# Optimization experiments

Hardware: AMD Instinct MI355X
Metric: run time of the kernel (lower is better)

Reference implementation:

```python
import jax, jax.numpy as jnp
import numpy as np

PATCH = 3      # forward default patch_size
ALPHA = 1.0    # forward default alpha
# scale_factor = 1 -> F.interpolate is the identity


def setup_inputs() -> dict:
    key = jax.random.key(0)
    x_l = jax.random.normal(key, (16, 1, 1536, 1536), dtype=jnp.float32)
    return {"x_l": x_l}


def reference(x_l):
    # x_l: [N, 1, H, W]
    N, C, H, W = x_l.shape
    p = PATCH
    pad = p // 2
    # zero-padded input, matching F.unfold's implicit zero padding
    xp = jnp.pad(x_l, ((0, 0), (0, 0), (pad, pad), (pad, pad)))
    # gather the p*p shifted views -> [N, p*p, H, W] (equivalent to F.unfold for C=1;
    # softmax + weighted sum over dim 1 is permutation-invariant over the patch axis)
    local = jnp.stack(
        [xp[:, 0, i:i + H, j:j + W] for i in range(p) for j in range(p)],
        axis=1,
    )
    # local_difference = local_l - x_l**2  (broadcast over the patch dim)
    diff = local - x_l[:, 0][:, None, :, :] ** 2
    corr = jax.nn.softmax(-diff / ALPHA, axis=1)
    # softmax-weighted local average -> [N, 1, H, W]
    return jnp.sum(corr * local, axis=1, keepdims=True)
```

## Files before the change

kernel.cpp:

```cpp
#include <hip/hip_runtime.h>
#include <math.h>

#define IMG_W 1536
#define IMG_H 1536
#define NIMG  16
#define RPB   32
#define NROWS (RPB + 2)
#define PF    6

typedef float f32x4 __attribute__((ext_vector_type(4)));

__global__ __launch_bounds__(128)
void WeightedAverage_55551107006568_kernel(const float* __restrict__ x,
                                           float* __restrict__ out) {
    const int g  = blockIdx.x * 128 + threadIdx.x;
    const int w0 = g << 2;
    const int h0 = blockIdx.y * RPB;
    const size_t plane = (size_t)blockIdx.z * ((size_t)IMG_H * IMG_W);
    const float* xp = x + plane;
    float* op = out + plane;

    const bool lok = (w0 > 0);
    const bool rok = (w0 + 4 < IMG_W);
    const int offL = lok ? -4 : 0;
    const int offR = rok ? 16 : 0;

    f32x4 m[NROWS];
    float hl[NROWS], hr[NROWS];

    auto issue = [&](int i) {
        const int r  = h0 - 1 + i;
        const int rc = r < 0 ? 0 : (r >= IMG_H ? IMG_H - 1 : r);
        const float* rp = xp + (size_t)rc * IMG_W + w0;
        m[i]  = *(const f32x4*)rp;
        hl[i] = *(const float*)((const char*)rp + offL);
        hr[i] = *(const float*)((const char*)rp + offR);
    };

#pragma unroll
    for (int i = 0; i < PF; ++i) issue(i);
    __builtin_amdgcn_sched_barrier(0);

    float hE[3][4], hVE[3][4];
#pragma unroll
    for (int i = 0; i < NROWS; ++i) {
        if (i + PF < NROWS) issue(i + PF);
        __builtin_amdgcn_sched_barrier(0);

        const int r  = h0 - 1 + i;
        const bool rv = (r >= 0) && (r < IMG_H);
        const int s = i % 3;

        f32x4 mm = m[i];
        float hlv = (rv && lok) ? hl[i] : 0.f;
        float hrv = (rv && rok) ? hr[i] : 0.f;
        if (!rv) mm = (f32x4){0.f, 0.f, 0.f, 0.f};

        const float eL = __expf(-hlv),  vL = hlv * eL;
        const float e0 = __expf(-mm.x), v0 = mm.x * e0;
        const float e1 = __expf(-mm.y), v1 = mm.y * e1;
        const float e2 = __expf(-mm.z), v2 = mm.z * e2;
        const float e3 = __expf(-mm.w), v3 = mm.w * e3;
        const float eR = __expf(-hrv),  vR = hrv * eR;
        hE[s][0] = eL + e0 + e1;  hVE[s][0] = vL + v0 + v1;
        hE[s][1] = e0 + e1 + e2;  hVE[s][1] = v0 + v1 + v2;
        hE[s][2] = e1 + e2 + e3;  hVE[s][2] = v1 + v2 + v3;
        hE[s][3] = e2 + e3 + eR;  hVE[s][3] = v2 + v3 + vR;

        if (i >= 2) {
            const int ro = h0 + i - 2;
            f32x4 o;
#pragma unroll
            for (int p = 0; p < 4; ++p) {
                const float den = hE[0][p] + hE[1][p] + hE[2][p];
                const float num = hVE[0][p] + hVE[1][p] + hVE[2][p];
                o[p] = __fdividef(num, den);
            }
            __builtin_nontemporal_store(o, (f32x4*)(op + (size_t)ro * IMG_W + w0));
        }
    }
}

extern "C" void kernel_launch(void* const* d_in, const int* in_sizes, int n_in,
                              void* d_out, int out_size, void* d_ws, size_t ws_size,
                              hipStream_t stream) {
    const float* x = (const float*)d_in[0];
    float* out = (float*)d_out;
    dim3 grid(IMG_W / (128 * 4), IMG_H / RPB, NIMG);
    dim3 block(128, 1, 1);
    WeightedAverage_55551107006568_kernel<<<grid, block, 0, stream>>>(x, out);
}
```

Before: 263.0 us.

## Stage row tiles in LDS via async global_load_lds with XCD-aware block mapping

Each block now copies a 10-row by 512-column tile plus halo columns into shared memory with direct global-to-LDS loads, replacing the per-thread register prefetch pipeline and its redundant scalar halo loads. Horizontal neighbours come from wave shuffles, and only the wave edge lanes read halos from LDS. Rows per block drop from 32 to 8, so vertical halo re-reads go up. A flattened 1D grid maps images to XCDs for L2 locality, and stores become ordinary rather than nontemporal.

```diff
diff --git a/kernel.cpp b/kernel.cpp
--- a/kernel.cpp
+++ b/kernel.cpp
@@ -4,64 +4,89 @@
 #define IMG_W 1536
 #define IMG_H 1536
 #define NIMG  16
-#define RPB   32
-#define NROWS (RPB + 2)
-#define PF    6
+#define RPB   8
+#define NRW   (RPB + 2)
+#define TCOLS 512
+#define LROW  520
 
 typedef float f32x4 __attribute__((ext_vector_type(4)));
 
-__global__ __launch_bounds__(128)
+__global__ __launch_bounds__(128, 4)
 void WeightedAverage_55551107006568_kernel(const float* __restrict__ x,
                                            float* __restrict__ out) {
-    const int g  = blockIdx.x * 128 + threadIdx.x;
-    const int w0 = g << 2;
-    const int h0 = blockIdx.y * RPB;
-    const size_t plane = (size_t)blockIdx.z * ((size_t)IMG_H * IMG_W);
+    __shared__ float lds[NRW][LROW];
+
+    const int bid   = blockIdx.x;
+    const int xcd   = bid & 7;
+    const int chunk = bid >> 3;
+    const int z     = (xcd << 1) + (chunk / 576);
+    const int rem   = chunk % 576;
+    const int yb    = rem / 3;
+    const int xb    = rem - yb * 3;
+    const int h0    = yb * RPB;
+    const int c0blk = xb * TCOLS;
+
+    const int tid  = threadIdx.x;
+    const int lane = tid & 63;
+    const int wid  = tid >> 6;
+    const size_t plane = (size_t)z * ((size_t)IMG_H * IMG_W);
     const float* xp = x + plane;
     float* op = out + plane;
 
-    const bool lok = (w0 > 0);
-    const bool rok = (w0 + 4 < IMG_W);
-    const int offL = lok ? -4 : 0;
-    const int offR = rok ? 16 : 0;
+#pragma unroll
+    for (int i = 0; i < NRW; ++i) {
+        int r = h0 - 1 + i;
+        r = r < 0 ? 0 : (r >= IMG_H ? IMG_H - 1 : r);
+        const float* gp = xp + (size_t)r * IMG_W + c0blk + tid * 4;
+        float* lp = &lds[i][4] + wid * 256;
+        __builtin_amdgcn_global_load_lds(
+            (const __attribute__((address_space(1))) void*)gp,
+            (__attribute__((address_space(3))) void*)lp, 16, 0, 0);
+    }
+    if (tid < NRW) {
+        const int i = tid;
+        int r = h0 - 1 + i;
+        r = r < 0 ? 0 : (r >= IMG_H ? IMG_H - 1 : r);
+        float v = 0.f;
+        if (xb > 0) v = xp[(size_t)r * IMG_W + c0blk - 1];
+        lds[i][3] = v;
+    } else if (tid >= 32 && tid < 32 + NRW) {
+        const int i = tid - 32;
+        int r = h0 - 1 + i;
+        r = r < 0 ? 0 : (r >= IMG_H ? IMG_H - 1 : r);
+        float v = 0.f;
+        if (xb < 2) v = xp[(size_t)r * IMG_W + c0blk + TCOLS];
+        lds[i][LROW - 4] = v;
+    }
+    __syncthreads();
 
-    f32x4 m[NROWS];
-    float hl[NROWS], hr[NROWS];
-
-    auto issue = [&](int i) {
-        const int r  = h0 - 1 + i;
-        const int rc = r < 0 ? 0 : (r >= IMG_H ? IMG_H - 1 : r);
-        const float* rp = xp + (size_t)rc * IMG_W + w0;
-        m[i]  = *(const f32x4*)rp;
-        hl[i] = *(const float*)((const char*)rp + offL);
-        hr[i] = *(const float*)((const char*)rp + offR);
-    };
-
-#pragma unroll
-    for (int i = 0; i < PF; ++i) issue(i);
-    __builtin_amdgcn_sched_barrier(0);
-
+    const int cL = 4 + tid * 4;
     float hE[3][4], hVE[3][4];
 #pragma unroll
-    for (int i = 0; i < NROWS; ++i) {
-        if (i + PF < NROWS) issue(i + PF);
-        __builtin_amdgcn_sched_barrier(0);
-
+    for (int i = 0; i < NRW; ++i) {
         const int r  = h0 - 1 + i;
         const bool rv = (r >= 0) && (r < IMG_H);
         const int s = i % 3;
 
-        f32x4 mm = m[i];
-        float hlv = (rv && lok) ? hl[i] : 0.f;
-        float hrv = (rv && rok) ? hr[i] : 0.f;
-        if (!rv) mm = (f32x4){0.f, 0.f, 0.f, 0.f};
+        f32x4 mm = *(const f32x4*)&lds[i][cL];
+        float xl = 0.f, xr = 0.f;
+        if (lane == 0)  xl = lds[i][cL - 1];
+        if (lane == 63) xr = lds[i][cL + 4];
+        if (!rv) { mm = (f32x4){0.f,0.f,0.f,0.f}; xl = 0.f; xr = 0.f; }
 
-        const float eL = __expf(-hlv),  vL = hlv * eL;
         const float e0 = __expf(-mm.x), v0 = mm.x * e0;
         const float e1 = __expf(-mm.y), v1 = mm.y * e1;
         const float e2 = __expf(-mm.z), v2 = mm.z * e2;
         const float e3 = __expf(-mm.w), v3 = mm.w * e3;
-        const float eR = __expf(-hrv),  vR = hrv * eR;
+        const float el = __expf(-xl),   vl = xl * el;
+        const float er = __expf(-xr),   vr = xr * er;
+        const float e3s = __shfl_up(e3, 1),   v3s = __shfl_up(v3, 1);
+        const float e0s = __shfl_down(e0, 1), v0s = __shfl_down(v0, 1);
+        const float eL = (lane == 0)  ? el : e3s;
+        const float vL = (lane == 0)  ? vl : v3s;
+        const float eR = (lane == 63) ? er : e0s;
+        const float vR = (lane == 63) ? vr : v0s;
+
         hE[s][0] = eL + e0 + e1;  hVE[s][0] = vL + v0 + v1;
         hE[s][1] = e0 + e1 + e2;  hVE[s][1] = v0 + v1 + v2;
         hE[s][2] = e1 + e2 + e3;  hVE[s][2] = v1 + v2 + v3;
@@ -76,7 +101,7 @@
                 const float num = hVE[0][p] + hVE[1][p] + hVE[2][p];
                 o[p] = __fdividef(num, den);
             }
-            __builtin_nontemporal_store(o, (f32x4*)(op + (size_t)ro * IMG_W + w0));
+            *(f32x4*)(op + (size_t)ro * IMG_W + c0blk + tid * 4) = o;
         }
     }
 }
@@ -86,7 +111,7 @@
                               hipStream_t stream) {
     const float* x = (const float*)d_in[0];
     float* out = (float*)d_out;
-    dim3 grid(IMG_W / (128 * 4), IMG_H / RPB, NIMG);
+    dim3 grid(9216, 1, 1);
     dim3 block(128, 1, 1);
     WeightedAverage_55551107006568_kernel<<<grid, block, 0, stream>>>(x, out);
 }
```

Result: no change. 259.3 us (-1.4%).
